# Kernel tuning notes

Hardware: AMD Instinct MI355X
Metric: run time of the kernel (lower is better)

## Reference

```python
import jax, jax.numpy as jnp
import numpy as np

B, T, C, H = 8, 1024, 1024, 16
D = C // H  # head dim = 64

def setup_inputs() -> dict:
    key = jax.random.key(0)
    k1, k2, k3 = jax.random.split(key, 3)
    x = jax.random.normal(k1, (B, T, C), dtype=jnp.float32)
    W_attn = jax.random.normal(k2, (C, 3 * C), dtype=jnp.float32) * (1.0 / np.sqrt(C))
    W_proj = jax.random.normal(k3, (C, C), dtype=jnp.float32) * (1.0 / np.sqrt(C))
    # Llama RoPE frequencies: base^(-2i/D)
    omega = (10000.0 ** (-jnp.arange(0, D, 2, dtype=jnp.float32) / D))  # [D/2]
    return {"x": x, "W_attn": W_attn, "W_proj": W_proj, "omega": omega}

def _apply_rope(x, omega):
    # x: [B, T, H, D]; omega: [D/2]
    t = x.shape[1]
    ang = jnp.arange(t, dtype=x.dtype)[:, None] * omega[None, :]  # [T, D/2]
    cos = jnp.cos(ang)[None, :, None, :]  # [1, T, 1, D/2]
    sin = jnp.sin(ang)[None, :, None, :]
    d2 = x.shape[-1] // 2
    x1, x2 = x[..., :d2], x[..., d2:]
    return jnp.concatenate([x1 * cos - x2 * sin, x2 * cos + x1 * sin], axis=-1)

def reference(x, W_attn, W_proj, omega):
    b, t, c = x.shape
    qkv = jnp.einsum('btc,cd->btd', x, W_attn)  # fused QKV projection
    q, k, v = jnp.split(qkv, 3, axis=-1)
    q = q.reshape(b, t, H, D)
    k = k.reshape(b, t, H, D)
    v = v.reshape(b, t, H, D)
    q = _apply_rope(q, omega)
    k = _apply_rope(k, omega)
    # non-causal SDPA
    scale = 1.0 / jnp.sqrt(jnp.asarray(D, dtype=x.dtype))
    scores = jnp.einsum('bqhd,bkhd->bhqk', q, k) * scale
    probs = jax.nn.softmax(scores, axis=-1)
    y = jnp.einsum('bhqk,bkhd->bqhd', probs, v).reshape(b, t, c)
    return jnp.einsum('btc,cd->btd', y, W_proj)
```

## Files before the change

kernel.cpp:

```cpp
#include <hip/hip_runtime.h>
#include <stdint.h>


typedef __attribute__((ext_vector_type(8))) short short8;
typedef __attribute__((ext_vector_type(4))) short short4v;
typedef __attribute__((ext_vector_type(4))) float floatx4;

#define DEV static __device__ __forceinline__

DEV uint16_t f2bf(float f) {
  union { float f; uint32_t i; } v; v.f = f;
  uint32_t u = v.i;
  return (uint16_t)((u + 0x7fffu + ((u >> 16) & 1u)) >> 16);
}

DEV void async_load16(const uint16_t* g, uint16_t* l) {
  __builtin_amdgcn_global_load_lds(
      (const __attribute__((address_space(1))) void*)g,
      (__attribute__((address_space(3))) void*)l, 16, 0, 0);
}

__global__ __launch_bounds__(256) void convert_f32_bf16(
    const float* __restrict__ in, uint16_t* __restrict__ out) {
  const size_t base = ((size_t)blockIdx.x * 256 + threadIdx.x) * 8;
  floatx4 a = *(const floatx4*)(in + base);
  floatx4 b = *(const floatx4*)(in + base + 4);
  short8 s;
  s[0] = (short)f2bf(a[0]); s[1] = (short)f2bf(a[1]);
  s[2] = (short)f2bf(a[2]); s[3] = (short)f2bf(a[3]);
  s[4] = (short)f2bf(b[0]); s[5] = (short)f2bf(b[1]);
  s[6] = (short)f2bf(b[2]); s[7] = (short)f2bf(b[3]);
  *(short8*)(out + base) = s;
}

__global__ __launch_bounds__(256) void transpose_w(
    const float* __restrict__ in, uint16_t* __restrict__ out, int R, int Ccols) {
  __shared__ uint16_t tile[64][65];
  const int tx = threadIdx.x & 63, ty = threadIdx.x >> 6;
  const int c0 = blockIdx.x * 64, r0 = blockIdx.y * 64;
  #pragma unroll
  for (int i = 0; i < 64; i += 4)
    tile[ty + i][tx] = f2bf(in[(size_t)(r0 + ty + i) * Ccols + c0 + tx]);
  __syncthreads();
  #pragma unroll
  for (int i = 0; i < 64; i += 4)
    out[(size_t)(c0 + ty + i) * R + r0 + tx] = tile[tx][ty + i];
}

__global__ __launch_bounds__(256) void gemm_qkv(
    const uint16_t* __restrict__ A, const uint16_t* __restrict__ Bt,
    const float* __restrict__ omega,
    uint16_t* __restrict__ Qr, uint16_t* __restrict__ Kr, uint16_t* __restrict__ Vr) {
  __shared__ uint16_t As[128 * 64];
  __shared__ uint16_t Bs[128 * 64];
  const int tid = threadIdx.x;
  const int wave = tid >> 6, lane = tid & 63;
  const int l15 = lane & 15, quad = lane >> 4;
  const int row0 = blockIdx.y * 128, col0 = blockIdx.x * 128;
  const int wr = (wave >> 1) * 64, wc = (wave & 1) * 64;
  const int K = 1024;
  const int sw = l15 & 7;

  floatx4 acc[4][4];
  const floatx4 z4 = {0.f, 0.f, 0.f, 0.f};
  #pragma unroll
  for (int mi = 0; mi < 4; mi++)
    #pragma unroll
    for (int ni = 0; ni < 4; ni++) acc[mi][ni] = z4;

  for (int k0 = 0; k0 < K; k0 += 64) {
    __syncthreads();
    #pragma unroll
    for (int i = 0; i < 4; i++) {
      const int e = i * 256 + tid;
      const int r = e >> 3;
      const int j = (e & 7) ^ (r & 7);
      async_load16(A + (size_t)(row0 + r) * K + k0 + j * 8, As + e * 8);
      async_load16(Bt + (size_t)(col0 + r) * K + k0 + j * 8, Bs + e * 8);
    }
    __syncthreads();
    #pragma unroll
    for (int ks = 0; ks < 2; ks++) {
      short8 af[4], bfr[4];
      #pragma unroll
      for (int mi = 0; mi < 4; mi++)
        af[mi] = *(const short8*)(&As[(wr + mi * 16 + l15) * 64 +
                                      (((ks * 4 + quad) ^ sw) * 8)]);
      #pragma unroll
      for (int ni = 0; ni < 4; ni++)
        bfr[ni] = *(const short8*)(&Bs[(wc + ni * 16 + l15) * 64 +
                                       (((ks * 4 + quad) ^ sw) * 8)]);
      #pragma unroll
      for (int mi = 0; mi < 4; mi++)
        #pragma unroll
        for (int ni = 0; ni < 4; ni++)
          acc[mi][ni] = __builtin_amdgcn_mfma_f32_16x16x32_bf16(
              af[mi], bfr[ni], acc[mi][ni], 0, 0, 0);
    }
  }

  const int cblk = col0 + wc;
  const int region = cblk >> 10;
  const int h = (cblk & 1023) >> 6;
  const int b = row0 >> 10;
  const int tbase = (row0 & 1023) + wr;
  const size_t bh = (size_t)b * 16 + h;
  uint16_t* dst = (region == 0) ? Qr : (region == 1) ? Kr : Vr;

  if (region < 2) {
    const float w0 = omega[l15];
    const float w1 = omega[l15 + 16];
    const float scl = (region == 0) ? 0.125f : 1.0f;
    #pragma unroll
    for (int mi = 0; mi < 4; mi++)
      #pragma unroll
      for (int r = 0; r < 4; r++) {
        const int t = tbase + mi * 16 + quad * 4 + r;
        const size_t base = (bh * 1024 + t) * 64;
        {
          float s, c; sincosf((float)t * w0, &s, &c);
          float x1 = acc[mi][0][r], x2 = acc[mi][2][r];
          dst[base + l15]      = f2bf((x1 * c - x2 * s) * scl);
          dst[base + l15 + 32] = f2bf((x2 * c + x1 * s) * scl);
        }
        {
          float s, c; sincosf((float)t * w1, &s, &c);
          float x1 = acc[mi][1][r], x2 = acc[mi][3][r];
          dst[base + 16 + l15]      = f2bf((x1 * c - x2 * s) * scl);
          dst[base + 16 + l15 + 32] = f2bf((x2 * c + x1 * s) * scl);
        }
      }
  } else {
    #pragma unroll
    for (int mi = 0; mi < 4; mi++)
      #pragma unroll
      for (int ni = 0; ni < 4; ni++)
        #pragma unroll
        for (int r = 0; r < 4; r++) {
          const int t = tbase + mi * 16 + quad * 4 + r;
          dst[(bh * 1024 + t) * 64 + ni * 16 + l15] = f2bf(acc[mi][ni][r]);
        }
  }
}

__global__ __launch_bounds__(256) void transpose_v(
    const uint16_t* __restrict__ Vr, uint16_t* __restrict__ Vt) {
  __shared__ uint16_t vs[64][72];
  const int tid = threadIdx.x;
  const int tt = blockIdx.x & 15, bh = blockIdx.x >> 4;
  const int t0 = tt * 64;
  #pragma unroll
  for (int i = 0; i < 2; i++) {
    int v = tid + 256 * i;
    int tl = v >> 3, d8 = (v & 7) * 8;
    *(short8*)(&vs[tl][d8]) =
        *(const short8*)(Vr + ((size_t)bh * 1024 + t0 + tl) * 64 + d8);
  }
  __syncthreads();
  #pragma unroll
  for (int i = 0; i < 16; i++) {
    int e = tid + 256 * i;
    int d = e >> 6, tl = e & 63;
    Vt[((size_t)bh * 64 + d) * 1024 + t0 + tl] = vs[tl][d];
  }
}

__global__ __launch_bounds__(256) void gemm_out(
    const uint16_t* __restrict__ A, const uint16_t* __restrict__ Bt,
    float* __restrict__ Cmat, int M, int N, int K) {
  __shared__ uint16_t As[128 * 64];
  __shared__ uint16_t Bs[128 * 64];
  const int tid = threadIdx.x;
  const int wave = tid >> 6, lane = tid & 63;
  const int l15 = lane & 15, quad = lane >> 4;
  const int row0 = blockIdx.y * 128, col0 = blockIdx.x * 128;
  const int wr = (wave >> 1) * 64, wc = (wave & 1) * 64;
  const int sw = l15 & 7;

  floatx4 acc[4][4];
  const floatx4 z4 = {0.f, 0.f, 0.f, 0.f};
  #pragma unroll
  for (int mi = 0; mi < 4; mi++)
    #pragma unroll
    for (int ni = 0; ni < 4; ni++) acc[mi][ni] = z4;

  for (int k0 = 0; k0 < K; k0 += 64) {
    __syncthreads();
    #pragma unroll
    for (int i = 0; i < 4; i++) {
      const int e = i * 256 + tid;
      const int r = e >> 3;
      const int j = (e & 7) ^ (r & 7);
      async_load16(A + (size_t)(row0 + r) * K + k0 + j * 8, As + e * 8);
      async_load16(Bt + (size_t)(col0 + r) * K + k0 + j * 8, Bs + e * 8);
    }
    __syncthreads();
    #pragma unroll
    for (int ks = 0; ks < 2; ks++) {
      short8 af[4], bfr[4];
      #pragma unroll
      for (int mi = 0; mi < 4; mi++)
        af[mi] = *(const short8*)(&As[(wr + mi * 16 + l15) * 64 +
                                      (((ks * 4 + quad) ^ sw) * 8)]);
      #pragma unroll
      for (int ni = 0; ni < 4; ni++)
        bfr[ni] = *(const short8*)(&Bs[(wc + ni * 16 + l15) * 64 +
                                       (((ks * 4 + quad) ^ sw) * 8)]);
      #pragma unroll
      for (int mi = 0; mi < 4; mi++)
        #pragma unroll
        for (int ni = 0; ni < 4; ni++)
          acc[mi][ni] = __builtin_amdgcn_mfma_f32_16x16x32_bf16(
              af[mi], bfr[ni], acc[mi][ni], 0, 0, 0);
    }
  }
  #pragma unroll
  for (int mi = 0; mi < 4; mi++)
    #pragma unroll
    for (int ni = 0; ni < 4; ni++) {
      const int col = col0 + wc + ni * 16 + l15;
      #pragma unroll
      for (int r = 0; r < 4; r++) {
        const int row = row0 + wr + mi * 16 + quad * 4 + r;
        Cmat[(size_t)row * N + col] = acc[mi][ni][r];
      }
    }
}

#define FLD 72

__global__ __launch_bounds__(256) void flash_attn(
    const uint16_t* __restrict__ Qr, const uint16_t* __restrict__ Kr,
    const uint16_t* __restrict__ Vt, uint16_t* __restrict__ Y) {
  __shared__ uint16_t Ks[64 * FLD];
  __shared__ uint16_t Vs[64 * FLD];
  __shared__ uint16_t Ps[64 * FLD];
  const int tid = threadIdx.x;
  const int wv = tid >> 6, lane = tid & 63;
  const int l15 = lane & 15, quad = lane >> 4;
  const int qt = blockIdx.x & 15, bh = blockIdx.x >> 4;
  const int b = bh >> 4, h = bh & 15;
  const int q0 = qt * 64;
  const uint16_t* Qbh = Qr + (size_t)bh * 1024 * 64;
  const uint16_t* Kbh = Kr + (size_t)bh * 1024 * 64;
  const uint16_t* Vbh = Vt + (size_t)bh * 64 * 1024;

  short8 bq[2];
  #pragma unroll
  for (int ks = 0; ks < 2; ks++)
    bq[ks] = *(const short8*)(Qbh + (size_t)(q0 + wv * 16 + l15) * 64 + ks * 32 + quad * 8);

  float psum = 0.0f;
  const floatx4 z4 = {0.f, 0.f, 0.f, 0.f};
  floatx4 oacc[4];
  #pragma unroll
  for (int mi = 0; mi < 4; mi++) oacc[mi] = z4;

  for (int kt = 0; kt < 16; kt++) {
    __syncthreads();
    #pragma unroll
    for (int i = 0; i < 2; i++) {
      int v = tid + 256 * i;
      int r = v >> 3, c8 = (v & 7) * 8;
      *(short8*)(&Ks[r * FLD + c8]) =
          *(const short8*)(Kbh + (size_t)(kt * 64 + r) * 64 + c8);
      *(short8*)(&Vs[r * FLD + c8]) =
          *(const short8*)(Vbh + (size_t)r * 1024 + kt * 64 + c8);
    }
    __syncthreads();

    floatx4 sacc[4];
    #pragma unroll
    for (int ni = 0; ni < 4; ni++) {
      sacc[ni] = z4;
      #pragma unroll
      for (int ks = 0; ks < 2; ks++) {
        short8 ak = *(const short8*)(&Ks[(ni * 16 + l15) * FLD + ks * 32 + quad * 8]);
        sacc[ni] = __builtin_amdgcn_mfma_f32_16x16x32_bf16(ak, bq[ks], sacc[ni], 0, 0, 0);
      }
    }

    #pragma unroll
    for (int ni = 0; ni < 4; ni++) {
      short4v pk;
      #pragma unroll
      for (int r = 0; r < 4; r++) {
        float p = __expf(sacc[ni][r]);
        psum += p;
        pk[r] = (short)f2bf(p);
      }
      *(short4v*)(&Ps[(wv * 16 + l15) * FLD + ni * 16 + quad * 4]) = pk;
    }

    short8 bp[2];
    #pragma unroll
    for (int ks = 0; ks < 2; ks++)
      bp[ks] = *(const short8*)(&Ps[(wv * 16 + l15) * FLD + ks * 32 + quad * 8]);
    #pragma unroll
    for (int mi = 0; mi < 4; mi++) {
      #pragma unroll
      for (int ks = 0; ks < 2; ks++) {
        short8 av = *(const short8*)(&Vs[(mi * 16 + l15) * FLD + ks * 32 + quad * 8]);
        oacc[mi] = __builtin_amdgcn_mfma_f32_16x16x32_bf16(av, bp[ks], oacc[mi], 0, 0, 0);
      }
    }
  }

  float l_tot = psum;
  l_tot += __shfl_xor(l_tot, 16, 64);
  l_tot += __shfl_xor(l_tot, 32, 64);
  const float linv = 1.0f / l_tot;

  const int t = q0 + wv * 16 + l15;
  #pragma unroll
  for (int mi = 0; mi < 4; mi++) {
    short4v yk;
    #pragma unroll
    for (int r = 0; r < 4; r++) yk[r] = (short)f2bf(oacc[mi][r] * linv);
    *(short4v*)(Y + (size_t)(b * 1024 + t) * 1024 + h * 64 + mi * 16 + quad * 4) = yk;
  }
}

extern "C" void kernel_launch(void* const* d_in, const int* in_sizes, int n_in,
                              void* d_out, int out_size, void* d_ws, size_t ws_size,
                              hipStream_t stream) {
  const float* x      = (const float*)d_in[0];
  const float* W_attn = (const float*)d_in[1];
  const float* W_proj = (const float*)d_in[2];
  const float* omega  = (const float*)d_in[3];
  float* out = (float*)d_out;

  uint16_t* wsp     = (uint16_t*)d_ws;
  uint16_t* xb      = wsp;
  uint16_t* Wt_attn = xb + (size_t)8192 * 1024;
  uint16_t* Wt_proj = Wt_attn + (size_t)3072 * 1024;
  uint16_t* Qr      = Wt_proj + (size_t)1024 * 1024;
  uint16_t* Kr      = Qr + (size_t)128 * 1024 * 64;
  uint16_t* Vr      = Kr + (size_t)128 * 1024 * 64;
  uint16_t* Vt      = xb;
  uint16_t* Y       = Vr;

  convert_f32_bf16<<<4096, 256, 0, stream>>>(x, xb);
  transpose_w<<<dim3(48, 16), 256, 0, stream>>>(W_attn, Wt_attn, 1024, 3072);
  transpose_w<<<dim3(16, 16), 256, 0, stream>>>(W_proj, Wt_proj, 1024, 1024);
  gemm_qkv<<<dim3(24, 64), 256, 0, stream>>>(xb, Wt_attn, omega, Qr, Kr, Vr);
  transpose_v<<<2048, 256, 0, stream>>>(Vr, Vt);
  flash_attn<<<2048, 256, 0, stream>>>(Qr, Kr, Vt, Y);
  gemm_out<<<dim3(8, 64), 256, 0, stream>>>(Y, Wt_proj, out, 8192, 1024, 1024);
}
```

Measured before the change: 284.5 us.

## Precompute RoPE sin/cos table and double query rows per flash-attention block

A small kernel now precomputes a cos/sin table over (t, freq), which the QKV GEMM epilogue reads instead of calling sincosf per element. Flash attention now processes 128 query rows per block (two 16-row groups per wave), so each K/V tile loaded into shared memory is reused twice as much and the grid is halved. Block order is also changed to put bh innermost. The trade-offs are more registers per wave, a larger P buffer in shared memory, fewer blocks to fill the GPU, and an extra kernel launch plus table reads.

```diff
diff --git a/kernel.cpp b/kernel.cpp
--- a/kernel.cpp
+++ b/kernel.cpp
@@ -33,6 +33,15 @@
   *(short8*)(out + base) = s;
 }
 
+__global__ __launch_bounds__(256) void rope_table(
+    const float* __restrict__ omega, float2* __restrict__ tab) {
+  const int idx = blockIdx.x * 256 + threadIdx.x;
+  const int t = idx >> 5, d = idx & 31;
+  float s, c;
+  sincosf((float)t * omega[d], &s, &c);
+  tab[idx] = make_float2(c, s);
+}
+
 __global__ __launch_bounds__(256) void transpose_w(
     const float* __restrict__ in, uint16_t* __restrict__ out, int R, int Ccols) {
   __shared__ uint16_t tile[64][65];
@@ -49,7 +58,7 @@
 
 __global__ __launch_bounds__(256) void gemm_qkv(
     const uint16_t* __restrict__ A, const uint16_t* __restrict__ Bt,
-    const float* __restrict__ omega,
+    const float2* __restrict__ tab,
     uint16_t* __restrict__ Qr, uint16_t* __restrict__ Kr, uint16_t* __restrict__ Vr) {
   __shared__ uint16_t As[128 * 64];
   __shared__ uint16_t Bs[128 * 64];
@@ -108,8 +117,6 @@
   uint16_t* dst = (region == 0) ? Qr : (region == 1) ? Kr : Vr;
 
   if (region < 2) {
-    const float w0 = omega[l15];
-    const float w1 = omega[l15 + 16];
     const float scl = (region == 0) ? 0.125f : 1.0f;
     #pragma unroll
     for (int mi = 0; mi < 4; mi++)
@@ -117,17 +124,17 @@
       for (int r = 0; r < 4; r++) {
         const int t = tbase + mi * 16 + quad * 4 + r;
         const size_t base = (bh * 1024 + t) * 64;
+        const float2 cs0 = tab[t * 32 + l15];
+        const float2 cs1 = tab[t * 32 + l15 + 16];
         {
-          float s, c; sincosf((float)t * w0, &s, &c);
           float x1 = acc[mi][0][r], x2 = acc[mi][2][r];
-          dst[base + l15]      = f2bf((x1 * c - x2 * s) * scl);
-          dst[base + l15 + 32] = f2bf((x2 * c + x1 * s) * scl);
+          dst[base + l15]      = f2bf((x1 * cs0.x - x2 * cs0.y) * scl);
+          dst[base + l15 + 32] = f2bf((x2 * cs0.x + x1 * cs0.y) * scl);
         }
         {
-          float s, c; sincosf((float)t * w1, &s, &c);
           float x1 = acc[mi][1][r], x2 = acc[mi][3][r];
-          dst[base + 16 + l15]      = f2bf((x1 * c - x2 * s) * scl);
-          dst[base + 16 + l15 + 32] = f2bf((x2 * c + x1 * s) * scl);
+          dst[base + 16 + l15]      = f2bf((x1 * cs1.x - x2 * cs1.y) * scl);
+          dst[base + 16 + l15 + 32] = f2bf((x2 * cs1.x + x1 * cs1.y) * scl);
         }
       }
   } else {
@@ -234,27 +241,32 @@
     const uint16_t* __restrict__ Vt, uint16_t* __restrict__ Y) {
   __shared__ uint16_t Ks[64 * FLD];
   __shared__ uint16_t Vs[64 * FLD];
-  __shared__ uint16_t Ps[64 * FLD];
+  __shared__ uint16_t Ps[128 * FLD];
   const int tid = threadIdx.x;
   const int wv = tid >> 6, lane = tid & 63;
   const int l15 = lane & 15, quad = lane >> 4;
-  const int qt = blockIdx.x & 15, bh = blockIdx.x >> 4;
+  const int bh = blockIdx.x & 127, qt = blockIdx.x >> 7;
   const int b = bh >> 4, h = bh & 15;
-  const int q0 = qt * 64;
+  const int q0 = qt * 128;
   const uint16_t* Qbh = Qr + (size_t)bh * 1024 * 64;
   const uint16_t* Kbh = Kr + (size_t)bh * 1024 * 64;
   const uint16_t* Vbh = Vt + (size_t)bh * 64 * 1024;
 
-  short8 bq[2];
-  #pragma unroll
-  for (int ks = 0; ks < 2; ks++)
-    bq[ks] = *(const short8*)(Qbh + (size_t)(q0 + wv * 16 + l15) * 64 + ks * 32 + quad * 8);
-
-  float psum = 0.0f;
+  short8 bq[2][2];
+  #pragma unroll
+  for (int g = 0; g < 2; g++)
+    #pragma unroll
+    for (int ks = 0; ks < 2; ks++)
+      bq[g][ks] = *(const short8*)(Qbh +
+          (size_t)(q0 + wv * 32 + g * 16 + l15) * 64 + ks * 32 + quad * 8);
+
+  float psum[2] = {0.f, 0.f};
   const floatx4 z4 = {0.f, 0.f, 0.f, 0.f};
-  floatx4 oacc[4];
-  #pragma unroll
-  for (int mi = 0; mi < 4; mi++) oacc[mi] = z4;
+  floatx4 oacc[2][4];
+  #pragma unroll
+  for (int g = 0; g < 2; g++)
+    #pragma unroll
+    for (int mi = 0; mi < 4; mi++) oacc[g][mi] = z4;
 
   for (int kt = 0; kt < 16; kt++) {
     __syncthreads();
@@ -269,55 +281,59 @@
     }
     __syncthreads();
 
-    floatx4 sacc[4];
-    #pragma unroll
-    for (int ni = 0; ni < 4; ni++) {
-      sacc[ni] = z4;
-      #pragma unroll
-      for (int ks = 0; ks < 2; ks++) {
-        short8 ak = *(const short8*)(&Ks[(ni * 16 + l15) * FLD + ks * 32 + quad * 8]);
-        sacc[ni] = __builtin_amdgcn_mfma_f32_16x16x32_bf16(ak, bq[ks], sacc[ni], 0, 0, 0);
-      }
-    }
-
-    #pragma unroll
-    for (int ni = 0; ni < 4; ni++) {
-      short4v pk;
-      #pragma unroll
-      for (int r = 0; r < 4; r++) {
-        float p = __expf(sacc[ni][r]);
-        psum += p;
-        pk[r] = (short)f2bf(p);
-      }
-      *(short4v*)(&Ps[(wv * 16 + l15) * FLD + ni * 16 + quad * 4]) = pk;
-    }
-
-    short8 bp[2];
-    #pragma unroll
-    for (int ks = 0; ks < 2; ks++)
-      bp[ks] = *(const short8*)(&Ps[(wv * 16 + l15) * FLD + ks * 32 + quad * 8]);
+    #pragma unroll
+    for (int g = 0; g < 2; g++) {
+      const int qrow = wv * 32 + g * 16 + l15;
+      floatx4 sacc[4];
+      #pragma unroll
+      for (int ni = 0; ni < 4; ni++) {
+        sacc[ni] = z4;
+        #pragma unroll
+        for (int ks = 0; ks < 2; ks++) {
+          short8 ak = *(const short8*)(&Ks[(ni * 16 + l15) * FLD + ks * 32 + quad * 8]);
+          sacc[ni] = __builtin_amdgcn_mfma_f32_16x16x32_bf16(ak, bq[g][ks], sacc[ni], 0, 0, 0);
+        }
+      }
+      #pragma unroll
+      for (int ni = 0; ni < 4; ni++) {
+        short4v pk;
+        #pragma unroll
+        for (int r = 0; r < 4; r++) {
+          float p = __expf(sacc[ni][r]);
+          psum[g] += p;
+          pk[r] = (short)f2bf(p);
+        }
+        *(short4v*)(&Ps[qrow * FLD + ni * 16 + quad * 4]) = pk;
+      }
+      short8 bp[2];
+      #pragma unroll
+      for (int ks = 0; ks < 2; ks++)
+        bp[ks] = *(const short8*)(&Ps[qrow * FLD + ks * 32 + quad * 8]);
+      #pragma unroll
+      for (int mi = 0; mi < 4; mi++) {
+        #pragma unroll
+        for (int ks = 0; ks < 2; ks++) {
+          short8 av = *(const short8*)(&Vs[(mi * 16 + l15) * FLD + ks * 32 + quad * 8]);
+          oacc[g][mi] = __builtin_amdgcn_mfma_f32_16x16x32_bf16(av, bp[ks], oacc[g][mi], 0, 0, 0);
+        }
+      }
+    }
+  }
+
+  #pragma unroll
+  for (int g = 0; g < 2; g++) {
+    float l_tot = psum[g];
+    l_tot += __shfl_xor(l_tot, 16, 64);
+    l_tot += __shfl_xor(l_tot, 32, 64);
+    const float linv = 1.0f / l_tot;
+    const int t = q0 + wv * 32 + g * 16 + l15;
     #pragma unroll
     for (int mi = 0; mi < 4; mi++) {
-      #pragma unroll
-      for (int ks = 0; ks < 2; ks++) {
-        short8 av = *(const short8*)(&Vs[(mi * 16 + l15) * FLD + ks * 32 + quad * 8]);
-        oacc[mi] = __builtin_amdgcn_mfma_f32_16x16x32_bf16(av, bp[ks], oacc[mi], 0, 0, 0);
-      }
-    }
-  }
-
-  float l_tot = psum;
-  l_tot += __shfl_xor(l_tot, 16, 64);
-  l_tot += __shfl_xor(l_tot, 32, 64);
-  const float linv = 1.0f / l_tot;
-
-  const int t = q0 + wv * 16 + l15;
-  #pragma unroll
-  for (int mi = 0; mi < 4; mi++) {
-    short4v yk;
-    #pragma unroll
-    for (int r = 0; r < 4; r++) yk[r] = (short)f2bf(oacc[mi][r] * linv);
-    *(short4v*)(Y + (size_t)(b * 1024 + t) * 1024 + h * 64 + mi * 16 + quad * 4) = yk;
+      short4v yk;
+      #pragma unroll
+      for (int r = 0; r < 4; r++) yk[r] = (short)f2bf(oacc[g][mi][r] * linv);
+      *(short4v*)(Y + (size_t)(b * 1024 + t) * 1024 + h * 64 + mi * 16 + quad * 4) = yk;
+    }
   }
 }
 
@@ -337,14 +353,16 @@
   uint16_t* Qr      = Wt_proj + (size_t)1024 * 1024;
   uint16_t* Kr      = Qr + (size_t)128 * 1024 * 64;
   uint16_t* Vr      = Kr + (size_t)128 * 1024 * 64;
+  float2*   ropet   = (float2*)(Vr + (size_t)128 * 1024 * 64);
   uint16_t* Vt      = xb;
   uint16_t* Y       = Vr;
 
   convert_f32_bf16<<<4096, 256, 0, stream>>>(x, xb);
+  rope_table<<<128, 256, 0, stream>>>(omega, ropet);
   transpose_w<<<dim3(48, 16), 256, 0, stream>>>(W_attn, Wt_attn, 1024, 3072);
   transpose_w<<<dim3(16, 16), 256, 0, stream>>>(W_proj, Wt_proj, 1024, 1024);
-  gemm_qkv<<<dim3(24, 64), 256, 0, stream>>>(xb, Wt_attn, omega, Qr, Kr, Vr);
+  gemm_qkv<<<dim3(24, 64), 256, 0, stream>>>(xb, Wt_attn, ropet, Qr, Kr, Vr);
   transpose_v<<<2048, 256, 0, stream>>>(Vr, Vt);
-  flash_attn<<<2048, 256, 0, stream>>>(Qr, Kr, Vt, Y);
+  flash_attn<<<1024, 256, 0, stream>>>(Qr, Kr, Vt, Y);
   gemm_out<<<dim3(8, 64), 256, 0, stream>>>(Y, Wt_proj, out, 8192, 1024, 1024);
 }
```

Result: faster. 278.4 us (-2.1%).
